# Kernel optimization log

Measured on AMD Instinct MI355X. Metric: run time of the kernel, lower is better.

## Reference

```python
import jax, jax.numpy as jnp
import numpy as np

N, C, K, B, G = 32768, 128, 16, 4, 8
SCALE, BASE = 2.0, 10000.0

def _bn(x, gamma, beta, eps=1e-5):
    # torch BatchNorm1d (training): stats over all axes except channel (last)
    axes = tuple(range(x.ndim - 1))
    mean = x.mean(axes)
    var = x.var(axes)
    return (x - mean) / jnp.sqrt(var + eps) * gamma + beta

def _cayley_rope(x, coord, S_param):
    c = x.shape[-1]
    S = jnp.triu(S_param, 1)
    S = S - S.T
    I = jnp.eye(c, dtype=x.dtype)
    P = jnp.linalg.solve(I + S, I - S)  # (I+S)^-1 (I-S)
    xr = x @ P.T
    dpa = c // 3 // 2 * 2          # dim per axis (even)
    dr = dpa * 3                   # rotated dims
    inv_freq = 1.0 / (BASE ** (jnp.arange(0, dpa, 2, dtype=jnp.float32) / dpa))
    cs = coord * SCALE
    def rot(f, c1):
        ang = c1[:, None] * inv_freq[None, :]
        s, co = jnp.sin(ang), jnp.cos(ang)
        fr, fi = jnp.split(f, 2, axis=-1)
        return jnp.concatenate([fr * co - fi * s, fr * s + fi * co], -1)
    parts = [rot(xr[:, i * dpa:(i + 1) * dpa], cs[:, i]) for i in range(3)]
    out = jnp.concatenate(parts + [xr[:, dr:]], -1)
    return out @ P

def setup_inputs() -> dict:
    key = jax.random.key(0)
    ks = jax.random.split(key, 24)
    w = lambda k, i, o, s=0.02: jax.random.normal(k, (i, o), jnp.float32) * s
    inp = {
        'feat': jax.random.normal(ks[0], (N, C), jnp.float32),
        'coord': jax.random.uniform(ks[1], (N, 3), jnp.float32) * 10.0,
        'reference_index': jax.random.randint(ks[2], (N, K), 0, N),
        'offset': jnp.arange(1, B + 1, dtype=jnp.int32) * (N // B),
        'Wq': w(ks[3], C, C), 'bq': jnp.zeros((C,)),
        'gq': jnp.ones((C,)), 'bnq': jnp.zeros((C,)),
        'Wk': w(ks[4], C, C), 'bk': jnp.zeros((C,)),
        'gk': jnp.ones((C,)), 'bnk': jnp.zeros((C,)),
        'Wv': w(ks[5], C, C), 'bv': jnp.zeros((C,)),
        'S_param': jax.random.normal(ks[6], (C, C), jnp.float32) * 0.01,
        'Ww1': w(ks[7], C, G), 'bw1': jnp.zeros((G,)),
        'gw': jnp.ones((G,)), 'bnw': jnp.zeros((G,)),
        'Ww2': w(ks[8], G, G), 'bw2': jnp.zeros((G,)),
        'Wg1': w(ks[9], 2 * C, C), 'bg1': jnp.zeros((C,)),
        'gg': jnp.ones((C,)), 'bng': jnp.zeros((C,)),
        'Wg2': w(ks[10], C, G, 0.001), 'bg2': jnp.full((G,), 3.0),
    }
    return inp

def reference(feat, coord, reference_index, offset, Wq, bq, gq, bnq, Wk, bk, gk, bnk,
              Wv, bv, S_param, Ww1, bw1, gw, bnw, Ww2, bw2, Wg1, bg1, gg, bng, Wg2, bg2):
    q_raw = jax.nn.relu(_bn(feat @ Wq + bq, gq, bnq))
    k_raw = jax.nn.relu(_bn(feat @ Wk + bk, gk, bnk))
    value = feat @ Wv + bv
    q = _cayley_rope(q_raw, coord, S_param)
    k = _cayley_rope(k_raw, coord, S_param)
    kg = k[reference_index]            # [N,K,C] gather
    vg = value[reference_index]        # [N,K,C]
    rel = kg - q[:, None, :]
    geom = jax.nn.relu(_bn(rel @ Ww1 + bw1, gw, bnw)) @ Ww2 + bw2  # [N,K,G]
    seg = jnp.searchsorted(offset, jnp.arange(N), side='right')
    gmax = jax.ops.segment_max(q_raw, seg, num_segments=B)
    gate_in = jnp.concatenate([q_raw, gmax[seg]], -1)              # [N,2C]
    gate = jax.nn.sigmoid(jax.nn.relu(_bn(gate_in @ Wg1 + bg1, gg, bng)) @ Wg2 + bg2)  # [N,G]
    refined = geom * (1.0 + gate[:, None, :])
    attn = jax.nn.softmax(refined, axis=1)
    mask = jnp.sign(reference_index + 1).astype(attn.dtype)
    attn = attn * mask[:, :, None]
    vg4 = vg.reshape(N, K, G, C // G)
    out = jnp.einsum('nkgi,nkg->ngi', vg4, attn).reshape(N, C)
    return out
```

## Files before the change

### kernel.cpp

```cpp
#include <hip/hip_runtime.h>
#include <math.h>

#define N_PTS 32768
#define C_DIM 128
#define K_NB  16
#define G_DIM 8

#define OF_PW     0
#define OF_STATQ  1024
#define OF_STATK  1280
#define OF_STATG1 1536
#define OF_STATH  1792
#define OF_UMAXP  1808
#define OF_UMAXN  2320
#define OF_WQT    4096
#define OF_WKT    12288
#define OF_WVT    20480
#define OF_WG1T   28672
#define OF_PTMIT  36864
#define OF_QW     65536
#define OF_KW     327680
#define OF_GATE   589824
#define OF_G1     1048576
#define OF_V      5242880

typedef short bf16x8 __attribute__((ext_vector_type(8)));
typedef float f32x4  __attribute__((ext_vector_type(4)));

#define LSTR 136
#define BSTR 132

__device__ __forceinline__ unsigned f2bf(float f) {
  unsigned u = __float_as_uint(f);
  return (u + 0x7fffu + ((u >> 16) & 1u)) >> 16;
}
__device__ __forceinline__ float bf2f(short s) {
  return __uint_as_float(((unsigned)(unsigned short)s) << 16);
}
__device__ __forceinline__ unsigned fenc(float f) {
  unsigned b = __float_as_uint(f);
  return (b & 0x80000000u) ? ~b : (b | 0x80000000u);
}
__device__ __forceinline__ float fdec(unsigned u) {
  unsigned b = (u & 0x80000000u) ? (u & 0x7fffffffu) : ~u;
  return __uint_as_float(b);
}
__device__ __forceinline__ bf16x8 pack_bf8(float4 a, float4 b) {
  bf16x8 r;
  r[0] = (short)f2bf(a.x); r[1] = (short)f2bf(a.y);
  r[2] = (short)f2bf(a.z); r[3] = (short)f2bf(a.w);
  r[4] = (short)f2bf(b.x); r[5] = (short)f2bf(b.y);
  r[6] = (short)f2bf(b.z); r[7] = (short)f2bf(b.w);
  return r;
}
__device__ __forceinline__ float fetch_asym(const float* M, int r, int c) {
  return (c > r) ? M[r*128 + c] : ((c < r) ? -M[c*128 + r] : 0.f);
}

__device__ __forceinline__ void stageB(short* dst, const short* __restrict__ src, int tid) {
  #pragma unroll
  for (int it = 0; it < 8; ++it) {
    int q = it*256 + tid;
    int r = q >> 4, c8 = q & 15;
    *(uint4*)&dst[r*BSTR + c8*8] = *(const uint4*)&src[r*128 + c8*8];
  }
}

__device__ __forceinline__ void gemm8_lds(const short* Bl, const bf16x8* af,
                                          f32x4* out, int l15, int quad)
{
  #pragma unroll
  for (int nt = 0; nt < 8; ++nt) {
    f32x4 ac = {0.f, 0.f, 0.f, 0.f};
    #pragma unroll
    for (int ks = 0; ks < 4; ++ks) {
      bf16x8 bf = *(const bf16x8*)&Bl[(nt*16 + l15)*BSTR + ks*32 + quad*8];
      ac = __builtin_amdgcn_mfma_f32_16x16x32_bf16(af[ks], bf, ac, 0, 0, 0);
    }
    out[nt] = ac;
  }
}

__global__ __launch_bounds__(256) void cayley(const float* __restrict__ Sp,
    const float* __restrict__ Ww1,
    const float* __restrict__ Wq, const float* __restrict__ Wk,
    const float* __restrict__ Wv, const float* __restrict__ Wg1,
    short* __restrict__ WqT, short* __restrict__ WkT,
    short* __restrict__ WvT, short* __restrict__ Wg1T,
    short* __restrict__ PTmIT, float* __restrict__ PW,
    float* __restrict__ statz)
{
  __shared__ short Ssh[128*LSTR];
  __shared__ float x0[128], x1[128];
  int bx = blockIdx.x, tid = threadIdx.x;
  if (bx >= 64) {
    if (bx < 80) {
      int idx = bx - 64, widx = idx >> 2, qr = idx & 3;
      const float* src = (widx == 0) ? Wq : (widx == 1) ? Wk : (widx == 2) ? Wv : Wg1;
      short* dst = (widx == 0) ? WqT : (widx == 1) ? WkT : (widx == 2) ? WvT : Wg1T;
      const float4* s4 = (const float4*)src;
      #pragma unroll
      for (int it = 0; it < 4; ++it) {
        int q = it*256 + tid; int k = qr*32 + (q >> 5), n4 = q & 31;
        float4 v = s4[k*32 + n4];
        dst[(n4*4+0)*128 + k] = (short)f2bf(v.x);
        dst[(n4*4+1)*128 + k] = (short)f2bf(v.y);
        dst[(n4*4+2)*128 + k] = (short)f2bf(v.z);
        dst[(n4*4+3)*128 + k] = (short)f2bf(v.w);
      }
    } else {
      #pragma unroll
      for (int it = 0; it < 8; ++it) {
        int idx = it*256 + tid;
        if (idx < 1808) statz[idx] = 0.f;
      }
    }
    return;
  }
  int c0 = bx*2, c1 = c0 + 1;
  #pragma unroll 8
  for (int it = 0; it < 64; ++it) {
    int idx = it*256 + tid; int i = idx >> 7, j = idx & 127;
    Ssh[i*LSTR + j] = (short)f2bf(fetch_asym(Sp, i, j));
  }
  if (tid < 128) {
    x0[tid] = (tid == c0) ? 1.f : 0.f;
    x1[tid] = (tid == c1) ? 1.f : 0.f;
  }
  __syncthreads();
  int i = tid >> 1, h = tid & 1;
  const short* srow = &Ssh[i*LSTR + h*64];
  for (int t = 0; t < 16; ++t) {
    float a0 = 0.f, a1 = 0.f;
    #pragma unroll
    for (int jq = 0; jq < 16; ++jq) {
      short4 sv = *(const short4*)&srow[jq*4];
      #pragma unroll
      for (int u = 0; u < 4; ++u) {
        float s = bf2f((&sv.x)[u]);
        int j = h*64 + jq*4 + u;
        a0 = fmaf(s, x0[j], a0);
        a1 = fmaf(s, x1[j], a1);
      }
    }
    a0 += __shfl_xor(a0, 1);
    a1 += __shfl_xor(a1, 1);
    __syncthreads();
    if (h == 0) {
      x0[i] = a0 + ((i == c0) ? 1.f : 0.f);
      x1[i] = a1 + ((i == c1) ? 1.f : 0.f);
    }
    __syncthreads();
  }
  if (tid < 128) {
    PTmIT[c0*128 + tid] = (short)f2bf(2.f*x0[tid] - ((tid == c0) ? 2.f : 0.f));
  } else {
    int t = tid - 128;
    PTmIT[c1*128 + t] = (short)f2bf(2.f*x1[t] - ((t == c1) ? 2.f : 0.f));
  }
  if (tid < 16) {
    int cc = tid >> 3, g = tid & 7;
    const float* xv = cc ? x1 : x0;
    int c = cc ? c1 : c0;
    float acc = 0.f;
    #pragma unroll 8
    for (int j = 0; j < 128; ++j) acc = fmaf(xv[j], Ww1[j*8 + g], acc);
    PW[c*8 + g] = 2.f*acc - Ww1[c*8 + g];
  }
}

__global__ __launch_bounds__(256, 2) void qkv_mfma(const float* __restrict__ feat,
    const short* __restrict__ WqT, const short* __restrict__ WkT, const short* __restrict__ WvT,
    const float* __restrict__ bq, const float* __restrict__ bk, const float* __restrict__ bv,
    float* __restrict__ Vv, float* __restrict__ Qlin, float* Klin,
    float* __restrict__ statq, float* __restrict__ statk,
    unsigned* __restrict__ umaxp, unsigned* __restrict__ umaxn)
{
  __shared__ short Bb0[128*BSTR];
  __shared__ short Bb1[128*BSTR];
  __shared__ float ssum[2][128], ssq[2][128];
  __shared__ unsigned ump[128], umn[128];
  int tid = threadIdx.x, row0 = blockIdx.x * 64, seg = row0 >> 13;
  if (tid < 128) {
    ssum[0][tid] = 0.f; ssum[1][tid] = 0.f;
    ssq[0][tid] = 0.f;  ssq[1][tid] = 0.f;
    ump[tid] = 0u; umn[tid] = 0u;
  }
  int lane = tid & 63, w = tid >> 6, l15 = lane & 15, quad = lane >> 4;
  stageB(Bb0, WqT, tid);
  bf16x8 af[4];
  {
    long rbase = (long)(row0 + w*16 + l15) * 128;
    #pragma unroll
    for (int ks = 0; ks < 4; ++ks) {
      int c0 = ks*32 + quad*8;
      float4 v0 = *(const float4*)&feat[rbase + c0];
      float4 v1 = *(const float4*)&feat[rbase + c0 + 4];
      af[ks] = pack_bf8(v0, v1);
    }
  }
  __syncthreads();
  stageB(Bb1, WkT, tid);
  {
    f32x4 acc8[8];
    gemm8_lds(Bb0, af, acc8, l15, quad);
    #pragma unroll
    for (int nt = 0; nt < 8; ++nt) {
      int col = nt*16 + l15;
      float bb = bq[col];
      float s = 0.f, s2 = 0.f, mx = -1e30f, mn = 1e30f;
      #pragma unroll
      for (int r = 0; r < 4; ++r) {
        float raw = acc8[nt][r];
        Qlin[(long)(row0 + w*16 + quad*4 + r)*128 + col] = raw;
        float v = raw + bb;
        s += v; s2 = fmaf(v, v, s2); mx = fmaxf(mx, v); mn = fminf(mn, v);
      }
      s += __shfl_xor(s, 16); s += __shfl_xor(s, 32);
      s2 += __shfl_xor(s2, 16); s2 += __shfl_xor(s2, 32);
      mx = fmaxf(mx, __shfl_xor(mx, 16)); mx = fmaxf(mx, __shfl_xor(mx, 32));
      mn = fminf(mn, __shfl_xor(mn, 16)); mn = fminf(mn, __shfl_xor(mn, 32));
      if (lane < 16) {
        atomicAdd(&ssum[0][col], s); atomicAdd(&ssq[0][col], s2);
        atomicMax(&ump[col], fenc(mx)); atomicMax(&umn[col], fenc(-mn));
      }
    }
  }
  __syncthreads();
  stageB(Bb0, WvT, tid);
  {
    f32x4 acc8[8];
    gemm8_lds(Bb1, af, acc8, l15, quad);
    #pragma unroll
    for (int nt = 0; nt < 8; ++nt) {
      int col = nt*16 + l15;
      float bb = bk[col];
      float s = 0.f, s2 = 0.f;
      #pragma unroll
      for (int r = 0; r < 4; ++r) {
        float raw = acc8[nt][r];
        Klin[(long)(row0 + w*16 + quad*4 + r)*128 + col] = raw;
        float v = raw + bb;
        s += v; s2 = fmaf(v, v, s2);
      }
      s += __shfl_xor(s, 16); s += __shfl_xor(s, 32);
      s2 += __shfl_xor(s2, 16); s2 += __shfl_xor(s2, 32);
      if (lane < 16) { atomicAdd(&ssum[1][col], s); atomicAdd(&ssq[1][col], s2); }
    }
  }
  __syncthreads();
  {
    f32x4 acc8[8];
    gemm8_lds(Bb0, af, acc8, l15, quad);
    #pragma unroll
    for (int nt = 0; nt < 8; ++nt) {
      int col = nt*16 + l15;
      float bb = bv[col];
      #pragma unroll
      for (int r = 0; r < 4; ++r)
        Vv[(long)(row0 + w*16 + quad*4 + r)*128 + col] = acc8[nt][r] + bb;
    }
  }
  __syncthreads();
  if (tid < 128) {
    atomicAdd(&statq[tid], ssum[0][tid]); atomicAdd(&statq[128 + tid], ssq[0][tid]);
    atomicAdd(&statk[tid], ssum[1][tid]); atomicAdd(&statk[128 + tid], ssq[1][tid]);
    atomicMax(&umaxp[seg*128 + tid], ump[tid]);
    atomicMax(&umaxn[seg*128 + tid], umn[tid]);
  }
}

__global__ __launch_bounds__(256, 3) void rqkw(
    const float* __restrict__ qlin, const float* klin,
    const short* __restrict__ PTmIT, const short* __restrict__ Wg1T,
    const float* __restrict__ coord,
    const float* __restrict__ bq, const float* __restrict__ bk,
    const float* __restrict__ statq, const float* __restrict__ statk,
    const float* __restrict__ gq, const float* __restrict__ bnq,
    const float* __restrict__ gk, const float* __restrict__ bnk,
    const unsigned* __restrict__ umaxp, const unsigned* __restrict__ umaxn,
    const float* __restrict__ Wg1, const float* __restrict__ bg1,
    const float* __restrict__ PW, const float* __restrict__ bw1,
    float* __restrict__ qw, float* __restrict__ kw,
    float* g1, float* __restrict__ statg1)
{
  __shared__ __align__(16) char arena[33792];
  __shared__ float pws[1024];
  __shared__ float caq[128], cbq[128], cak[128], cbk[128];
  __shared__ float gml[128], gsg[128];
  __shared__ float ssum[128], ssq[128];
  short* Bbuf = (short*)arena;
  float* xsq = (float*)arena;
  float* xsk = (float*)(arena + 16896);
  int tid = threadIdx.x;
  int row0 = blockIdx.x * 32, seg = row0 >> 13;
  const float invn = 1.f / 32768.f;
  if (tid < 128) {
    float m = statq[tid]*invn, vv = fmaf(-m, m, statq[128 + tid]*invn);
    float a = rsqrtf(vv + 1e-5f) * gq[tid];
    float b = fmaf(-m, a, bnq[tid]);
    caq[tid] = a; cbq[tid] = fmaf(a, bq[tid], b);
    float mx = fdec(umaxp[seg*128 + tid]);
    float mn = -fdec(umaxn[seg*128 + tid]);
    gml[tid] = fmaxf(0.f, fmaxf(fmaf(a, mx, b), fmaf(a, mn, b)));
    m = statk[tid]*invn; vv = fmaf(-m, m, statk[128 + tid]*invn);
    a = rsqrtf(vv + 1e-5f) * gk[tid];
    b = fmaf(-m, a, bnk[tid]);
    cak[tid] = a; cbk[tid] = fmaf(a, bk[tid], b);
    ssum[tid] = 0.f; ssq[tid] = 0.f;
  }
  #pragma unroll
  for (int it = 0; it < 4; ++it) { int idx = it*256 + tid; pws[idx] = PW[idx]; }
  stageB(Bbuf, PTmIT, tid);
  __syncthreads();
  int lane = tid & 63, w = tid >> 6, l15 = lane & 15, quad = lane >> 4;
  bool isq = (w < 2);
  int rw = (w & 1) * 16;
  const float* ca = isq ? caq : cak;
  const float* cb = isq ? cbq : cbk;
  const float* lin = isq ? qlin : klin;
  float rawd[32];
  #pragma unroll
  for (int nt = 0; nt < 8; ++nt) {
    int col = nt*16 + l15;
    long rb = (long)(row0 + rw + quad*4)*128 + col;
    #pragma unroll
    for (int r = 0; r < 4; ++r)
      rawd[nt*4 + r] = lin[rb + (long)r*128];
  }
  bf16x8 af2[4];
  #pragma unroll
  for (int ks = 0; ks < 4; ++ks) {
    int c0 = ks*32 + quad*8;
    const float* lp = &lin[(long)(row0 + rw + l15)*128 + c0];
    float4 v0 = *(const float4*)lp;
    float4 v1 = *(const float4*)(lp + 4);
    float4 b0, b1;
    b0.x = fmaxf(0.f, fmaf(ca[c0+0], v0.x, cb[c0+0]));
    b0.y = fmaxf(0.f, fmaf(ca[c0+1], v0.y, cb[c0+1]));
    b0.z = fmaxf(0.f, fmaf(ca[c0+2], v0.z, cb[c0+2]));
    b0.w = fmaxf(0.f, fmaf(ca[c0+3], v0.w, cb[c0+3]));
    b1.x = fmaxf(0.f, fmaf(ca[c0+4], v1.x, cb[c0+4]));
    b1.y = fmaxf(0.f, fmaf(ca[c0+5], v1.y, cb[c0+5]));
    b1.z = fmaxf(0.f, fmaf(ca[c0+6], v1.z, cb[c0+6]));
    b1.w = fmaxf(0.f, fmaf(ca[c0+7], v1.w, cb[c0+7]));
    af2[ks] = pack_bf8(b0, b1);
  }
  f32x4 accv[8];
  gemm8_lds(Bbuf, af2, accv, l15, quad);
  __syncthreads();
  stageB(Bbuf, Wg1T, tid);
  __syncthreads();
  f32x4 accw[8];
  if (isq) {
    gemm8_lds(Bbuf, af2, accw, l15, quad);
  } else {
    int c = tid - 128;
    float acc = bg1[c];
    #pragma unroll 8
    for (int j = 0; j < 128; ++j)
      acc = fmaf(gml[j], Wg1[(128 + j)*128 + c], acc);
    gsg[c] = acc;
  }
  float bnl[32];
  #pragma unroll
  for (int nt = 0; nt < 8; ++nt) {
    int col = nt*16 + l15;
    float A = ca[col], B = cb[col];
    #pragma unroll
    for (int r = 0; r < 4; ++r)
      bnl[nt*4 + r] = fmaxf(0.f, fmaf(A, rawd[nt*4 + r], B));
  }
  __syncthreads();
  {
    float* xs = isq ? xsq : xsk;
    #pragma unroll
    for (int nt = 0; nt < 8; ++nt) {
      int col = nt*16 + l15;
      #pragma unroll
      for (int r = 0; r < 4; ++r)
        xs[(rw + quad*4 + r)*132 + col] = accv[nt][r] + bnl[nt*4 + r];
    }
  }
  if (isq) {
    #pragma unroll
    for (int nt = 0; nt < 8; ++nt) {
      int col = nt*16 + l15;
      float gsv = gsg[col];
      float s = 0.f, s2 = 0.f;
      #pragma unroll
      for (int r = 0; r < 4; ++r) {
        float v = accw[nt][r] + gsv;
        g1[(long)(row0 + rw + quad*4 + r)*128 + col] = v;
        s += v; s2 = fmaf(v, v, s2);
      }
      s += __shfl_xor(s, 16); s += __shfl_xor(s, 32);
      s2 += __shfl_xor(s2, 16); s2 += __shfl_xor(s2, 32);
      if (lane < 16) { atomicAdd(&ssum[col], s); atomicAdd(&ssq[col], s2); }
    }
  }
  __syncthreads();
  if (tid < 128) {
    atomicAdd(&statg1[tid], ssum[tid]);
    atomicAdd(&statg1[128 + tid], ssq[tid]);
  }
  #pragma unroll
  for (int it = 0; it < 8; ++it) {
    int idx = it*256 + tid;
    int r = idx >> 6, s = idx & 63;
    if (s < 63) {
      int a3 = s / 21, j = s - a3*21;
      int cr = a3*42 + j;
      float invf = exp2f((float)(2*j) * (-13.287712379549449f / 42.f));
      float ang = coord[(row0 + r)*3 + a3] * (2.0f * invf);
      float sn, co; sincosf(ang, &sn, &co);
      float fr = xsq[r*132 + cr], fi = xsq[r*132 + cr + 21];
      xsq[r*132 + cr]      = fr*co - fi*sn;
      xsq[r*132 + cr + 21] = fr*sn + fi*co;
      fr = xsk[r*132 + cr]; fi = xsk[r*132 + cr + 21];
      xsk[r*132 + cr]      = fr*co - fi*sn;
      xsk[r*132 + cr + 21] = fr*sn + fi*co;
    }
  }
  __syncthreads();
  #pragma unroll
  for (int it = 0; it < 2; ++it) {
    int idx = it*256 + tid;
    int mat = idx >> 8, r2 = (idx >> 3) & 31, g = idx & 7;
    const float* x2 = mat ? xsk : xsq;
    float a0 = 0.f, a1 = 0.f, a2 = 0.f, a3 = 0.f;
    #pragma unroll 8
    for (int i = 0; i < 128; i += 4) {
      float4 xv = *(const float4*)&x2[r2*132 + i];
      a0 = fmaf(xv.x, pws[(i+0)*8 + g], a0);
      a1 = fmaf(xv.y, pws[(i+1)*8 + g], a1);
      a2 = fmaf(xv.z, pws[(i+2)*8 + g], a2);
      a3 = fmaf(xv.w, pws[(i+3)*8 + g], a3);
    }
    float acc = (a0 + a1) + (a2 + a3) + (mat ? bw1[g] : 0.f);
    float* dst = mat ? kw : qw;
    dst[(long)(row0 + r2)*8 + g] = acc;
  }
}

__global__ __launch_bounds__(256) void mid(
    const float* __restrict__ g1, const float* __restrict__ statg1,
    const float* __restrict__ ggm, const float* __restrict__ bng,
    const float* __restrict__ Wg2, const float* __restrict__ bg2,
    float* __restrict__ gate,
    const float* __restrict__ kw, const float* __restrict__ qw,
    const int* __restrict__ ref, float* __restrict__ stath)
{
  __shared__ float gs[32][132];
  __shared__ float w2s[128][8];
  __shared__ float cA[128], cB[128];
  __shared__ float red[256];
  int tid = threadIdx.x;
  if (blockIdx.x < 1024) {
    int row0 = blockIdx.x * 32;
    #pragma unroll
    for (int it = 0; it < 4; ++it) { int idx = tid + it*256; w2s[idx >> 3][idx & 7] = Wg2[idx]; }
    if (tid < 128) {
      const float invn = 1.f / 32768.f;
      float m = statg1[tid]*invn, v = fmaf(-m, m, statg1[128 + tid]*invn);
      float a = rsqrtf(v + 1e-5f) * ggm[tid];
      cA[tid] = a; cB[tid] = fmaf(-m, a, bng[tid]);
    }
    #pragma unroll
    for (int it = 0; it < 4; ++it) {
      int idx = tid + it*256; int r = idx >> 5, cq = idx & 31;
      *(float4*)&gs[r][cq*4] = *(const float4*)&g1[(long)(row0 + r)*128 + cq*4];
    }
    __syncthreads();
    int r = tid >> 3, g = tid & 7;
    float acc = bg2[g];
    #pragma unroll 8
    for (int c2 = 0; c2 < 128; ++c2) {
      float act = fmaxf(0.f, fmaf(gs[r][c2], cA[c2], cB[c2]));
      acc = fmaf(act, w2s[c2][g], acc);
    }
    gate[(long)(row0 + r)*8 + g] = 1.f / (1.f + expf(-acc));
  } else {
    long base = (long)(blockIdx.x - 1024) * 4096;
    float s = 0.f, sq = 0.f;
    for (int it = 0; it < 16; ++it) {
      long idx = base + it*256 + tid;
      int n = (int)(idx >> 7); int kk = (int)((idx >> 3) & 15); int g = (int)(idx & 7);
      int r = ref[n*16 + kk];
      float h = kw[(long)r*8 + g] - qw[(long)n*8 + g];
      s += h; sq = fmaf(h, h, sq);
    }
    red[tid] = s; __syncthreads();
    for (int d = 128; d >= 8; d >>= 1) { if (tid < d) red[tid] += red[tid + d]; __syncthreads(); }
    if (tid < 8) atomicAdd(&stath[tid], red[tid]);
    __syncthreads();
    red[tid] = sq; __syncthreads();
    for (int d = 128; d >= 8; d >>= 1) { if (tid < d) red[tid] += red[tid + d]; __syncthreads(); }
    if (tid < 8) atomicAdd(&stath[8 + tid], red[tid]);
  }
}

__global__ __launch_bounds__(256) void attn_out(const float* __restrict__ qw, const float* __restrict__ kw,
                                                const float* __restrict__ stath,
                                                const float* __restrict__ gw, const float* __restrict__ bnw,
                                                const float* __restrict__ Ww2, const float* __restrict__ bw2,
                                                const float* __restrict__ gate, const int* __restrict__ ref,
                                                const float* __restrict__ v, float* __restrict__ out)
{
  __shared__ float sm1[2][16][9];
  __shared__ float sm2[2][16][9];
  __shared__ int   smr[2][16];
  int tid = threadIdx.x; int rh = tid >> 7, t = tid & 127;
  int n = blockIdx.x * 2 + rh;
  int kk = t >> 3, g = t & 7;
  if (t < 16) smr[rh][t] = ref[n*16 + t];
  __syncthreads();
  const float invnk = 1.f / 524288.f;
  float m0 = stath[g]*invnk, v0 = fmaf(-m0, m0, stath[8 + g]*invnk);
  float aw = rsqrtf(v0 + 1e-5f) * gw[g];
  float bw = fmaf(-m0, aw, bnw[g]);
  int rr = smr[rh][kk];
  float h = kw[(long)rr*8 + g] - qw[(long)n*8 + g];
  sm1[rh][kk][g] = fmaxf(0.f, fmaf(h, aw, bw));
  __syncthreads();
  float acc = bw2[g];
  #pragma unroll
  for (int g2 = 0; g2 < 8; ++g2) acc = fmaf(sm1[rh][kk][g2], Ww2[g2*8 + g], acc);
  float refined = acc * (1.f + gate[(long)n*8 + g]);
  sm2[rh][kk][g] = refined;
  __syncthreads();
  float mx = -1e30f;
  #pragma unroll
  for (int k2 = 0; k2 < 16; ++k2) mx = fmaxf(mx, sm2[rh][k2][g]);
  float e = expf(refined - mx);
  sm1[rh][kk][g] = e;
  __syncthreads();
  float ssum = 0.f;
  #pragma unroll
  for (int k2 = 0; k2 < 16; ++k2) ssum += sm1[rh][k2][g];
  float mask = ((rr + 1) > 0) ? 1.f : (((rr + 1) == 0) ? 0.f : -1.f);
  float attn = e / ssum * mask;
  sm2[rh][kk][g] = attn;
  __syncthreads();
  float o = 0.f;
  #pragma unroll
  for (int k2 = 0; k2 < 16; ++k2) {
    o = fmaf(v[(long)smr[rh][k2]*128 + t], sm2[rh][k2][t >> 4], o);
  }
  out[(long)n*128 + t] = o;
}

extern "C" void kernel_launch(void* const* d_in, const int* in_sizes, int n_in,
                              void* d_out, int out_size, void* d_ws, size_t ws_size,
                              hipStream_t stream)
{
  const float* feat  = (const float*)d_in[0];
  const float* coord = (const float*)d_in[1];
  const int*   ref   = (const int*)d_in[2];
  const float* Wq  = (const float*)d_in[4];
  const float* bq  = (const float*)d_in[5];
  const float* gq  = (const float*)d_in[6];
  const float* bnq = (const float*)d_in[7];
  const float* Wk  = (const float*)d_in[8];
  const float* bk  = (const float*)d_in[9];
  const float* gk  = (const float*)d_in[10];
  const float* bnk = (const float*)d_in[11];
  const float* Wv  = (const float*)d_in[12];
  const float* bv  = (const float*)d_in[13];
  const float* Sp  = (const float*)d_in[14];
  const float* Ww1 = (const float*)d_in[15];
  const float* bw1 = (const float*)d_in[16];
  const float* gw  = (const float*)d_in[17];
  const float* bnw = (const float*)d_in[18];
  const float* Ww2 = (const float*)d_in[19];
  const float* bw2 = (const float*)d_in[20];
  const float* Wg1 = (const float*)d_in[21];
  const float* bg1 = (const float*)d_in[22];
  const float* ggm = (const float*)d_in[23];
  const float* bng = (const float*)d_in[24];
  const float* Wg2 = (const float*)d_in[25];
  const float* bg2 = (const float*)d_in[26];
  float* out = (float*)d_out;

  float* W = (float*)d_ws;
  float* PW = W + OF_PW;
  short* WqT   = (short*)(W + OF_WQT);
  short* WkT   = (short*)(W + OF_WKT);
  short* WvT   = (short*)(W + OF_WVT);
  short* Wg1T  = (short*)(W + OF_WG1T);
  short* PTmIT = (short*)(W + OF_PTMIT);
  float* G1 = W + OF_G1;
  float* Vv = W + OF_V;
  float* Qlin = (float*)d_out;
  float* Klin = G1;

  cayley<<<81, 256, 0, stream>>>(Sp, Ww1, Wq, Wk, Wv, Wg1,
                                 WqT, WkT, WvT, Wg1T, PTmIT, PW, W + OF_STATQ);
  qkv_mfma<<<512, 256, 0, stream>>>(feat, WqT, WkT, WvT, bq, bk, bv, Vv,
                                    Qlin, Klin,
                                    W + OF_STATQ, W + OF_STATK,
                                    (unsigned*)(W + OF_UMAXP), (unsigned*)(W + OF_UMAXN));
  rqkw<<<1024, 256, 0, stream>>>(Qlin, Klin, PTmIT, Wg1T, coord,
                                 bq, bk,
                                 W + OF_STATQ, W + OF_STATK,
                                 gq, bnq, gk, bnk,
                                 (const unsigned*)(W + OF_UMAXP), (const unsigned*)(W + OF_UMAXN),
                                 Wg1, bg1, PW, bw1,
                                 W + OF_QW, W + OF_KW, G1, W + OF_STATG1);
  mid<<<2048, 256, 0, stream>>>(G1, W + OF_STATG1, ggm, bng, Wg2, bg2, W + OF_GATE,
                                W + OF_KW, W + OF_QW, ref, W + OF_STATH);
  attn_out<<<16384, 256, 0, stream>>>(W + OF_QW, W + OF_KW, W + OF_STATH, gw, bnw, Ww2, bw2,
                                      W + OF_GATE, ref, Vv, out);
}
```

Before: 341.9 us.

## Stage GEMM weights via async global-to-LDS loads with XOR swizzle

Replaces the register-staged, padded LDS copies of the bf16 weight matrices with direct global_load_lds transfers into an unpadded, XOR-swizzled LDS layout. The MFMA reads use the matching swizzle, and each GEMM epilogue is fused per column tile so fewer accumulators stay live. In rqkw, occupancy is raised to 4 blocks, the LDS arena and row stride shrink, and block indices are remapped. The segment-max gate term is now computed inline from global memory, and the raw loads and weight staging start earlier. The 130-float stride makes float4 LDS reads misaligned for odd rows, and the inline gate loop adds global reads per thread.

```diff
diff --git a/kernel.cpp b/kernel.cpp
--- a/kernel.cpp
+++ b/kernel.cpp
@@ -28,7 +28,6 @@
 typedef float f32x4  __attribute__((ext_vector_type(4)));
 
 #define LSTR 136
-#define BSTR 132
 
 __device__ __forceinline__ unsigned f2bf(float f) {
   unsigned u = __float_as_uint(f);
@@ -57,24 +56,34 @@
   return (c > r) ? M[r*128 + c] : ((c < r) ? -M[c*128 + r] : 0.f);
 }
 
-__device__ __forceinline__ void stageB(short* dst, const short* __restrict__ src, int tid) {
+__device__ __forceinline__ void g2l16(const void* g, void* l) {
+  __builtin_amdgcn_global_load_lds(
+      (const __attribute__((address_space(1))) void*)g,
+      (__attribute__((address_space(3))) void*)l, 16, 0, 0);
+}
+
+__device__ __forceinline__ void stage_async(short* dst, const short* __restrict__ src, int tid) {
+  int lane = tid & 63, wv = tid >> 6;
   #pragma unroll
   for (int it = 0; it < 8; ++it) {
-    int q = it*256 + tid;
-    int r = q >> 4, c8 = q & 15;
-    *(uint4*)&dst[r*BSTR + c8*8] = *(const uint4*)&src[r*128 + c8*8];
-  }
-}
-
-__device__ __forceinline__ void gemm8_lds(const short* Bl, const bf16x8* af,
+    int chunk = it*256 + wv*64;
+    int D = (chunk + lane)*16;
+    int gs = D ^ (((D >> 8) & 7) << 4);
+    g2l16((const char*)src + gs, (char*)dst + chunk*16);
+  }
+}
+
+__device__ __forceinline__ void gemm8_swz(const short* Bb, const bf16x8* af,
                                           f32x4* out, int l15, int quad)
 {
+  int sx = (l15 & 7) << 4;
   #pragma unroll
   for (int nt = 0; nt < 8; ++nt) {
     f32x4 ac = {0.f, 0.f, 0.f, 0.f};
     #pragma unroll
     for (int ks = 0; ks < 4; ++ks) {
-      bf16x8 bf = *(const bf16x8*)&Bl[(nt*16 + l15)*BSTR + ks*32 + quad*8];
+      const char* p = (const char*)Bb + ((((nt*16 + l15)*256) + ks*64 + quad*16) ^ sx);
+      bf16x8 bf = *(const bf16x8*)p;
       ac = __builtin_amdgcn_mfma_f32_16x16x32_bf16(af[ks], bf, ac, 0, 0, 0);
     }
     out[nt] = ac;
@@ -176,18 +185,18 @@
     float* __restrict__ statq, float* __restrict__ statk,
     unsigned* __restrict__ umaxp, unsigned* __restrict__ umaxn)
 {
-  __shared__ short Bb0[128*BSTR];
-  __shared__ short Bb1[128*BSTR];
+  __shared__ __align__(16) short Bb0[128*128];
+  __shared__ __align__(16) short Bb1[128*128];
   __shared__ float ssum[2][128], ssq[2][128];
   __shared__ unsigned ump[128], umn[128];
   int tid = threadIdx.x, row0 = blockIdx.x * 64, seg = row0 >> 13;
+  int lane = tid & 63, w = tid >> 6, l15 = lane & 15, quad = lane >> 4;
+  stage_async(Bb0, WqT, tid);
   if (tid < 128) {
     ssum[0][tid] = 0.f; ssum[1][tid] = 0.f;
     ssq[0][tid] = 0.f;  ssq[1][tid] = 0.f;
     ump[tid] = 0u; umn[tid] = 0u;
   }
-  int lane = tid & 63, w = tid >> 6, l15 = lane & 15, quad = lane >> 4;
-  stageB(Bb0, WqT, tid);
   bf16x8 af[4];
   {
     long rbase = (long)(row0 + w*16 + l15) * 128;
@@ -200,21 +209,27 @@
     }
   }
   __syncthreads();
-  stageB(Bb1, WkT, tid);
+  stage_async(Bb1, WkT, tid);
   {
-    f32x4 acc8[8];
-    gemm8_lds(Bb0, af, acc8, l15, quad);
+    int sx = (l15 & 7) << 4;
     #pragma unroll
     for (int nt = 0; nt < 8; ++nt) {
+      f32x4 ac = {0.f, 0.f, 0.f, 0.f};
+      #pragma unroll
+      for (int ks = 0; ks < 4; ++ks) {
+        const char* p = (const char*)Bb0 + ((((nt*16 + l15)*256) + ks*64 + quad*16) ^ sx);
+        ac = __builtin_amdgcn_mfma_f32_16x16x32_bf16(af[ks], *(const bf16x8*)p, ac, 0, 0, 0);
+      }
       int col = nt*16 + l15;
       float bb = bq[col];
       float s = 0.f, s2 = 0.f, mx = -1e30f, mn = 1e30f;
       #pragma unroll
       for (int r = 0; r < 4; ++r) {
-        float raw = acc8[nt][r];
+        float raw = ac[r];
         Qlin[(long)(row0 + w*16 + quad*4 + r)*128 + col] = raw;
         float v = raw + bb;
-        s += v; s2 = fmaf(v, v, s2); mx = fmaxf(mx, v); mn = fminf(mn, v);
+        s += v; s2 = fmaf(v, v, s2);
+        mx = fmaxf(mx, raw); mn = fminf(mn, raw);
       }
       s += __shfl_xor(s, 16); s += __shfl_xor(s, 32);
       s2 += __shfl_xor(s2, 16); s2 += __shfl_xor(s2, 32);
@@ -227,18 +242,23 @@
     }
   }
   __syncthreads();
-  stageB(Bb0, WvT, tid);
+  stage_async(Bb0, WvT, tid);
   {
-    f32x4 acc8[8];
-    gemm8_lds(Bb1, af, acc8, l15, quad);
+    int sx = (l15 & 7) << 4;
     #pragma unroll
     for (int nt = 0; nt < 8; ++nt) {
+      f32x4 ac = {0.f, 0.f, 0.f, 0.f};
+      #pragma unroll
+      for (int ks = 0; ks < 4; ++ks) {
+        const char* p = (const char*)Bb1 + ((((nt*16 + l15)*256) + ks*64 + quad*16) ^ sx);
+        ac = __builtin_amdgcn_mfma_f32_16x16x32_bf16(af[ks], *(const bf16x8*)p, ac, 0, 0, 0);
+      }
       int col = nt*16 + l15;
       float bb = bk[col];
       float s = 0.f, s2 = 0.f;
       #pragma unroll
       for (int r = 0; r < 4; ++r) {
-        float raw = acc8[nt][r];
+        float raw = ac[r];
         Klin[(long)(row0 + w*16 + quad*4 + r)*128 + col] = raw;
         float v = raw + bb;
         s += v; s2 = fmaf(v, v, s2);
@@ -250,15 +270,20 @@
   }
   __syncthreads();
   {
-    f32x4 acc8[8];
-    gemm8_lds(Bb0, af, acc8, l15, quad);
+    int sx = (l15 & 7) << 4;
     #pragma unroll
     for (int nt = 0; nt < 8; ++nt) {
+      f32x4 ac = {0.f, 0.f, 0.f, 0.f};
+      #pragma unroll
+      for (int ks = 0; ks < 4; ++ks) {
+        const char* p = (const char*)Bb0 + ((((nt*16 + l15)*256) + ks*64 + quad*16) ^ sx);
+        ac = __builtin_amdgcn_mfma_f32_16x16x32_bf16(af[ks], *(const bf16x8*)p, ac, 0, 0, 0);
+      }
       int col = nt*16 + l15;
       float bb = bv[col];
       #pragma unroll
       for (int r = 0; r < 4; ++r)
-        Vv[(long)(row0 + w*16 + quad*4 + r)*128 + col] = acc8[nt][r] + bb;
+        Vv[(long)(row0 + w*16 + quad*4 + r)*128 + col] = ac[r] + bb;
     }
   }
   __syncthreads();
@@ -270,7 +295,7 @@
   }
 }
 
-__global__ __launch_bounds__(256, 3) void rqkw(
+__global__ __launch_bounds__(256, 4) void rqkw(
     const float* __restrict__ qlin, const float* klin,
     const short* __restrict__ PTmIT, const short* __restrict__ Wg1T,
     const float* __restrict__ coord,
@@ -284,25 +309,38 @@
     float* __restrict__ qw, float* __restrict__ kw,
     float* g1, float* __restrict__ statg1)
 {
-  __shared__ __align__(16) char arena[33792];
+  __shared__ __align__(16) char arena[33280];
   __shared__ float pws[1024];
   __shared__ float caq[128], cbq[128], cak[128], cbk[128];
-  __shared__ float gml[128], gsg[128];
+  __shared__ float gsg[128];
   __shared__ float ssum[128], ssq[128];
-  short* Bbuf = (short*)arena;
+  short* Bb = (short*)arena;
   float* xsq = (float*)arena;
-  float* xsk = (float*)(arena + 16896);
+  float* xsk = (float*)(arena + 16640);
   int tid = threadIdx.x;
-  int row0 = blockIdx.x * 32, seg = row0 >> 13;
+  int gb = blockIdx.x;
+  int c = ((((gb >> 4) << 3) | (gb & 7)) << 1) | ((gb >> 3) & 1);
+  int row0 = c * 32, seg = row0 >> 13;
+  int lane = tid & 63, w = tid >> 6, l15 = lane & 15, quad = lane >> 4;
+  bool isq = (w < 2);
+  int rw = (w & 1) * 16;
+  const float* lin = isq ? qlin : klin;
+  stage_async(Bb, PTmIT, tid);
+  float rawd[32];
+  #pragma unroll
+  for (int nt = 0; nt < 8; ++nt) {
+    int col = nt*16 + l15;
+    long rb = (long)(row0 + rw + quad*4)*128 + col;
+    #pragma unroll
+    for (int r = 0; r < 4; ++r)
+      rawd[nt*4 + r] = lin[rb + (long)r*128];
+  }
   const float invn = 1.f / 32768.f;
   if (tid < 128) {
     float m = statq[tid]*invn, vv = fmaf(-m, m, statq[128 + tid]*invn);
     float a = rsqrtf(vv + 1e-5f) * gq[tid];
     float b = fmaf(-m, a, bnq[tid]);
     caq[tid] = a; cbq[tid] = fmaf(a, bq[tid], b);
-    float mx = fdec(umaxp[seg*128 + tid]);
-    float mn = -fdec(umaxn[seg*128 + tid]);
-    gml[tid] = fmaxf(0.f, fmaxf(fmaf(a, mx, b), fmaf(a, mn, b)));
     m = statk[tid]*invn; vv = fmaf(-m, m, statk[128 + tid]*invn);
     a = rsqrtf(vv + 1e-5f) * gk[tid];
     b = fmaf(-m, a, bnk[tid]);
@@ -311,23 +349,9 @@
   }
   #pragma unroll
   for (int it = 0; it < 4; ++it) { int idx = it*256 + tid; pws[idx] = PW[idx]; }
-  stageB(Bbuf, PTmIT, tid);
-  __syncthreads();
-  int lane = tid & 63, w = tid >> 6, l15 = lane & 15, quad = lane >> 4;
-  bool isq = (w < 2);
-  int rw = (w & 1) * 16;
+  __syncthreads();
   const float* ca = isq ? caq : cak;
   const float* cb = isq ? cbq : cbk;
-  const float* lin = isq ? qlin : klin;
-  float rawd[32];
-  #pragma unroll
-  for (int nt = 0; nt < 8; ++nt) {
-    int col = nt*16 + l15;
-    long rb = (long)(row0 + rw + quad*4)*128 + col;
-    #pragma unroll
-    for (int r = 0; r < 4; ++r)
-      rawd[nt*4 + r] = lin[rb + (long)r*128];
-  }
   bf16x8 af2[4];
   #pragma unroll
   for (int ks = 0; ks < 4; ++ks) {
@@ -347,20 +371,21 @@
     af2[ks] = pack_bf8(b0, b1);
   }
   f32x4 accv[8];
-  gemm8_lds(Bbuf, af2, accv, l15, quad);
-  __syncthreads();
-  stageB(Bbuf, Wg1T, tid);
-  __syncthreads();
-  f32x4 accw[8];
-  if (isq) {
-    gemm8_lds(Bbuf, af2, accw, l15, quad);
-  } else {
-    int c = tid - 128;
-    float acc = bg1[c];
-    #pragma unroll 8
-    for (int j = 0; j < 128; ++j)
-      acc = fmaf(gml[j], Wg1[(128 + j)*128 + c], acc);
-    gsg[c] = acc;
+  gemm8_swz(Bb, af2, accv, l15, quad);
+  __syncthreads();
+  stage_async(Bb, Wg1T, tid);
+  if (!isq) {
+    int cgs = tid - 128;
+    float acc = bg1[cgs];
+    #pragma unroll 4
+    for (int j = 0; j < 128; ++j) {
+      float a = caq[j], b = cbq[j];
+      float mx = fdec(umaxp[seg*128 + j]);
+      float mn = -fdec(umaxn[seg*128 + j]);
+      float gmlj = fmaxf(0.f, fmaxf(fmaf(a, mx, b), fmaf(a, mn, b)));
+      acc = fmaf(gmlj, Wg1[(128 + j)*128 + cgs], acc);
+    }
+    gsg[cgs] = acc;
   }
   float bnl[32];
   #pragma unroll
@@ -372,25 +397,22 @@
       bnl[nt*4 + r] = fmaxf(0.f, fmaf(A, rawd[nt*4 + r], B));
   }
   __syncthreads();
-  {
-    float* xs = isq ? xsq : xsk;
+  if (isq) {
+    int sx = (l15 & 7) << 4;
     #pragma unroll
     for (int nt = 0; nt < 8; ++nt) {
-      int col = nt*16 + l15;
-      #pragma unroll
-      for (int r = 0; r < 4; ++r)
-        xs[(rw + quad*4 + r)*132 + col] = accv[nt][r] + bnl[nt*4 + r];
-    }
-  }
-  if (isq) {
-    #pragma unroll
-    for (int nt = 0; nt < 8; ++nt) {
+      f32x4 ac = {0.f, 0.f, 0.f, 0.f};
+      #pragma unroll
+      for (int ks = 0; ks < 4; ++ks) {
+        const char* p = (const char*)Bb + ((((nt*16 + l15)*256) + ks*64 + quad*16) ^ sx);
+        ac = __builtin_amdgcn_mfma_f32_16x16x32_bf16(af2[ks], *(const bf16x8*)p, ac, 0, 0, 0);
+      }
       int col = nt*16 + l15;
       float gsv = gsg[col];
       float s = 0.f, s2 = 0.f;
       #pragma unroll
       for (int r = 0; r < 4; ++r) {
-        float v = accw[nt][r] + gsv;
+        float v = ac[r] + gsv;
         g1[(long)(row0 + rw + quad*4 + r)*128 + col] = v;
         s += v; s2 = fmaf(v, v, s2);
       }
@@ -400,10 +422,21 @@
     }
   }
   __syncthreads();
+  {
+    float* xs = isq ? xsq : xsk;
+    #pragma unroll
+    for (int nt = 0; nt < 8; ++nt) {
+      int col = nt*16 + l15;
+      #pragma unroll
+      for (int r = 0; r < 4; ++r)
+        xs[(rw + quad*4 + r)*130 + col] = accv[nt][r] + bnl[nt*4 + r];
+    }
+  }
   if (tid < 128) {
     atomicAdd(&statg1[tid], ssum[tid]);
     atomicAdd(&statg1[128 + tid], ssq[tid]);
   }
+  __syncthreads();
   #pragma unroll
   for (int it = 0; it < 8; ++it) {
     int idx = it*256 + tid;
@@ -414,12 +447,12 @@
       float invf = exp2f((float)(2*j) * (-13.287712379549449f / 42.f));
       float ang = coord[(row0 + r)*3 + a3] * (2.0f * invf);
       float sn, co; sincosf(ang, &sn, &co);
-      float fr = xsq[r*132 + cr], fi = xsq[r*132 + cr + 21];
-      xsq[r*132 + cr]      = fr*co - fi*sn;
-      xsq[r*132 + cr + 21] = fr*sn + fi*co;
-      fr = xsk[r*132 + cr]; fi = xsk[r*132 + cr + 21];
-      xsk[r*132 + cr]      = fr*co - fi*sn;
-      xsk[r*132 + cr + 21] = fr*sn + fi*co;
+      float fr = xsq[r*130 + cr], fi = xsq[r*130 + cr + 21];
+      xsq[r*130 + cr]      = fr*co - fi*sn;
+      xsq[r*130 + cr + 21] = fr*sn + fi*co;
+      fr = xsk[r*130 + cr]; fi = xsk[r*130 + cr + 21];
+      xsk[r*130 + cr]      = fr*co - fi*sn;
+      xsk[r*130 + cr + 21] = fr*sn + fi*co;
     }
   }
   __syncthreads();
@@ -431,7 +464,7 @@
     float a0 = 0.f, a1 = 0.f, a2 = 0.f, a3 = 0.f;
     #pragma unroll 8
     for (int i = 0; i < 128; i += 4) {
-      float4 xv = *(const float4*)&x2[r2*132 + i];
+      float4 xv = *(const float4*)&x2[r2*130 + i];
       a0 = fmaf(xv.x, pws[(i+0)*8 + g], a0);
       a1 = fmaf(xv.y, pws[(i+1)*8 + g], a1);
       a2 = fmaf(xv.z, pws[(i+2)*8 + g], a2);
```

After: 395.1 us. +15.6%, slower.
